# Kernel tuning notes

Hardware: AMD Instinct MI355X
Metric: run time of the kernel (lower is better)

Reference implementation:

```python
import jax, jax.numpy as jnp
import numpy as np
from functools import partial

TAU = 2.0
EPS = 1e-5

@jax.custom_vjp
def spike(x):
    # Heaviside spike (x >= 0 -> 1). Surrogate sigmoid grad (alpha=4), matching spikingjelly default.
    return (x >= 0).astype(x.dtype)

def _spike_fwd(x):
    return (x >= 0).astype(x.dtype), x

def _spike_bwd(x, g):
    s = jax.nn.sigmoid(4.0 * x)
    return (4.0 * s * (1.0 - s) * g,)

spike.defvjp(_spike_fwd, _spike_bwd)

def lif(x, v_threshold=1.0):
    # Multi-step LIF over leading time axis. v_reset=0, hard reset, detach_reset.
    def step(v, xt):
        v = v + (xt - v) / TAU
        s = spike(v - v_threshold)
        v = v * (1.0 - jax.lax.stop_gradient(s))  # detached hard reset
        return v, s
    _, s = jax.lax.scan(step, jnp.zeros_like(x[0]), x)
    return s

def bn(x, gamma, beta):
    # BatchNorm1d in training mode over (T*B, C, N): stats over axes (T,B,N) per channel.
    m = x.mean(axis=(0, 1, 3), keepdims=True)
    v = x.var(axis=(0, 1, 3), keepdims=True)
    return (x - m) * jax.lax.rsqrt(v + EPS) * gamma[None, None, :, None] + beta[None, None, :, None]

def conv1x1(x, w, b=None):
    # 1x1 conv1d == channel-mixing GEMM. x: [T,B,C,N], w: [O,C]
    y = jnp.einsum('oc,tbcn->tbon', w, x)
    if b is not None:
        y = y + b[None, None, :, None]
    return y

def setup_inputs() -> dict:
    key = jax.random.key(0)
    ks = jax.random.split(key, 16)
    T, B, C, H, W = 4, 16, 512, 16, 16
    sc = 1.0 / np.sqrt(C)
    inp = {
        'x': jax.random.normal(ks[0], (T, B, C, H, W), dtype=jnp.float32),
        'q_w': jax.random.normal(ks[1], (C, C), dtype=jnp.float32) * sc,
        'q_gamma': jnp.ones((C,), jnp.float32), 'q_beta': jnp.zeros((C,), jnp.float32),
        'k_w': jax.random.normal(ks[2], (C, C), dtype=jnp.float32) * sc,
        'k_gamma': jnp.ones((C,), jnp.float32), 'k_beta': jnp.zeros((C,), jnp.float32),
        'v_w': jax.random.normal(ks[3], (C, C), dtype=jnp.float32) * sc,
        'v_gamma': jnp.ones((C,), jnp.float32), 'v_beta': jnp.zeros((C,), jnp.float32),
        'proj_w': jax.random.normal(ks[4], (C, C), dtype=jnp.float32) * sc,
        'proj_b': jnp.zeros((C,), jnp.float32),
        'proj_gamma': jnp.ones((C,), jnp.float32), 'proj_beta': jnp.zeros((C,), jnp.float32),
    }
    return inp

def reference(x, q_w, q_gamma, q_beta, k_w, k_gamma, k_beta, v_w, v_gamma, v_beta,
              proj_w, proj_b, proj_gamma, proj_beta):
    num_heads = 8
    scale = 0.125
    T, B, C, H, W = x.shape
    N = H * W
    d = C // num_heads
    xf = x.reshape(T, B, C, N)

    def branch(w, gamma, beta):
        s = lif(bn(conv1x1(xf, w), gamma, beta))          # [T,B,C,N] spikes
        # -> [T,B,heads,N,d]
        return s.transpose(0, 1, 3, 2).reshape(T, B, N, num_heads, d).transpose(0, 1, 3, 2, 4)

    q = branch(q_w, q_gamma, q_beta)
    k = branch(k_w, k_gamma, k_beta)
    v = branch(v_w, v_gamma, v_beta)

    kv = jnp.einsum('tbhnd,tbhne->tbhde', k, v)           # [T,B,h,d,d]
    attn = jnp.einsum('tbhnd,tbhde->tbhne', q, kv) * scale  # [T,B,h,N,d]
    attn = attn.transpose(0, 1, 2, 4, 3).reshape(T, B, C, N)
    attn = lif(attn, v_threshold=0.5)

    out = bn(conv1x1(attn, proj_w, proj_b), proj_gamma, proj_beta)
    out = lif(out.reshape(T, B, C, H, W))
    return out
```

## Files before the change

kernel.cpp:

```cpp
#include <hip/hip_runtime.h>
#include <stdint.h>

#define BCN  (16*512*256)
#define CN   (512*256)
#define NG   64

template<typename IN_T>
__global__ __launch_bounds__(256, 4)
void conv_gemm_v2(const IN_T* __restrict__ X, const float* __restrict__ W,
                  const float* __restrict__ bias, float* __restrict__ Y) {
  const int g  = blockIdx.z;
  const int o0 = blockIdx.y << 7;
  const int n0 = blockIdx.x << 6;
  const int tid = threadIdx.x;
  const int tx = tid & 15, ty = tid >> 4;

  const IN_T* __restrict__ Xg = X + (size_t)g * CN;
  float* __restrict__ Yg = Y + (size_t)g * CN;

  __shared__ double wS[128][33];
  __shared__ double xS[32][66];

  double acc[8][4] = {};

  float wst[16];
  float xst[8];

  auto loadW = [&](int c0) {
    #pragma unroll
    for (int i = 0; i < 4; ++i) {
      int L = i * 256 + tid;
      int o = L >> 3, c4 = (L & 7) << 2;
      const float4 v = *(const float4*)&W[(size_t)(o0 + o) * 512 + c0 + c4];
      wst[4*i+0] = v.x; wst[4*i+1] = v.y; wst[4*i+2] = v.z; wst[4*i+3] = v.w;
    }
  };
  auto loadX = [&](int c0) {
    #pragma unroll
    for (int i = 0; i < 2; ++i) {
      int L = i * 256 + tid;
      int c = L >> 4, n4 = (L & 15) << 2;
      if constexpr (sizeof(IN_T) == 4) {
        const float4 v = *(const float4*)&Xg[(size_t)(c0 + c) * 256 + n0 + n4];
        xst[4*i+0] = v.x; xst[4*i+1] = v.y; xst[4*i+2] = v.z; xst[4*i+3] = v.w;
      } else {
        const uchar4 v = *(const uchar4*)&Xg[(size_t)(c0 + c) * 256 + n0 + n4];
        xst[4*i+0] = (float)v.x; xst[4*i+1] = (float)v.y;
        xst[4*i+2] = (float)v.z; xst[4*i+3] = (float)v.w;
      }
    }
  };
  auto storeTiles = [&]() {
    #pragma unroll
    for (int i = 0; i < 4; ++i) {
      int L = i * 256 + tid;
      int o = L >> 3, c4 = (L & 7) << 2;
      #pragma unroll
      for (int u = 0; u < 4; ++u) wS[o][c4 + u] = (double)wst[4*i+u];
    }
    #pragma unroll
    for (int i = 0; i < 2; ++i) {
      int L = i * 256 + tid;
      int c = L >> 4, n4 = (L & 15) << 2;
      #pragma unroll
      for (int u = 0; u < 4; ++u) xS[c][n4 + u] = (double)xst[4*i+u];
    }
  };

  loadW(0); loadX(0);

  for (int c0 = 0; c0 < 512; c0 += 32) {
    __syncthreads();
    storeTiles();
    __syncthreads();
    if (c0 + 32 < 512) { loadW(c0 + 32); loadX(c0 + 32); }

    #pragma unroll
    for (int k = 0; k < 32; ++k) {
      double b[4];
      #pragma unroll
      for (int j = 0; j < 4; ++j) b[j] = xS[k][tx + 16*j];
      #pragma unroll
      for (int i = 0; i < 8; ++i) {
        double a = wS[ty*8 + i][k];
        #pragma unroll
        for (int j = 0; j < 4; ++j) acc[i][j] = fma(a, b[j], acc[i][j]);
      }
    }
  }

  #pragma unroll
  for (int i = 0; i < 8; ++i) {
    const int o = o0 + ty*8 + i;
    const double bi = bias ? (double)bias[o] : 0.0;
    #pragma unroll
    for (int j = 0; j < 4; ++j)
      Yg[(size_t)o * 256 + n0 + tx + 16*j] = (float)(acc[i][j] + bi);
  }
}

__global__ __launch_bounds__(256)
void bn_stats(const float* __restrict__ Y, const float* __restrict__ gamma,
              const float* __restrict__ beta, double* __restrict__ stats) {
  const int c = blockIdx.x;
  const int tid = threadIdx.x;
  __shared__ double redA[256];
  __shared__ double redB[256];

  double s = 0.0, s2 = 0.0;
  for (int g = 0; g < NG; ++g) {
    double y = (double)Y[((size_t)g * 512 + c) * 256 + tid];
    s += y; s2 += y * y;
  }
  redA[tid] = s; redB[tid] = s2; __syncthreads();
  for (int off = 128; off > 0; off >>= 1) {
    if (tid < off) { redA[tid] += redA[tid + off]; redB[tid] += redB[tid + off]; }
    __syncthreads();
  }
  if (tid == 0) {
    double m = redA[0] * (1.0 / 16384.0);
    double var = redB[0] * (1.0 / 16384.0) - m * m;
    double rstd = 1.0 / sqrt(var + 1e-5);
    double scale = (double)gamma[c] * rstd;
    stats[c] = scale;
    stats[512 + c] = (double)beta[c] - m * scale;
  }
}

__global__ __launch_bounds__(256)
void lif_kernel(const float* __restrict__ Y, const double* __restrict__ stats,
                double thresh, unsigned char* __restrict__ s_u8,
                float* __restrict__ s_f32) {
  const size_t idx = (size_t)blockIdx.x * 256 + threadIdx.x;
  const int c = (int)((idx >> 8) & 511);
  double scale = 1.0, shift = 0.0;
  if (stats) { scale = stats[c]; shift = stats[512 + c]; }
  double v = 0.0;
  #pragma unroll
  for (int t = 0; t < 4; ++t) {
    double z = (double)Y[(size_t)t * BCN + idx] * scale + shift;
    v = v + (z - v) * 0.5;
    bool sp = (v - thresh) >= 0.0;
    if (s_u8) s_u8[(size_t)t * BCN + idx] = sp ? 1 : 0;
    else      s_f32[(size_t)t * BCN + idx] = sp ? 1.0f : 0.0f;
    if (sp) v = 0.0;
  }
}

__global__ __launch_bounds__(256)
void attn_kv(const unsigned char* __restrict__ sk, const unsigned char* __restrict__ sv,
             float* __restrict__ kv) {
  const int blk = blockIdx.x;
  const int tid = threadIdx.x;
  const size_t base = ((size_t)(blk >> 3) * 512 + (size_t)(blk & 7) * 64) * 256;
  __shared__ unsigned char kS[64][256];
  __shared__ unsigned char vS[64][256];
  const uint32_t* K32 = (const uint32_t*)(sk + base);
  const uint32_t* V32 = (const uint32_t*)(sv + base);
  uint32_t* kS32 = (uint32_t*)&kS[0][0];
  uint32_t* vS32 = (uint32_t*)&vS[0][0];
  #pragma unroll
  for (int i = 0; i < 16; ++i) {
    kS32[i * 256 + tid] = K32[i * 256 + tid];
    vS32[i * 256 + tid] = V32[i * 256 + tid];
  }
  __syncthreads();
  const int d0 = (tid >> 4) << 2, e0 = (tid & 15) << 2;
  int acc[4][4] = {};
  for (int n = 0; n < 256; ++n) {
    int k_[4], v_[4];
    #pragma unroll
    for (int i = 0; i < 4; ++i) k_[i] = kS[d0 + i][n];
    #pragma unroll
    for (int j = 0; j < 4; ++j) v_[j] = vS[e0 + j][n];
    #pragma unroll
    for (int i = 0; i < 4; ++i)
      #pragma unroll
      for (int j = 0; j < 4; ++j) acc[i][j] += k_[i] * v_[j];
  }
  float* KV = kv + (size_t)blk * 4096;
  #pragma unroll
  for (int i = 0; i < 4; ++i)
    #pragma unroll
    for (int j = 0; j < 4; ++j)
      KV[(d0 + i) * 64 + e0 + j] = (float)acc[i][j];
}

__global__ __launch_bounds__(256)
void attn_qkv(const unsigned char* __restrict__ sq, const float* __restrict__ kv,
              float* __restrict__ attn) {
  const int blk = blockIdx.x;
  const int tid = threadIdx.x;
  const size_t base = ((size_t)(blk >> 3) * 512 + (size_t)(blk & 7) * 64) * 256;
  __shared__ unsigned char qS[64][256];
  __shared__ float kvS[64][64];
  const uint32_t* Q32 = (const uint32_t*)(sq + base);
  uint32_t* qS32 = (uint32_t*)&qS[0][0];
  const float* KV = kv + (size_t)blk * 4096;
  #pragma unroll
  for (int i = 0; i < 16; ++i) {
    qS32[i * 256 + tid] = Q32[i * 256 + tid];
    (&kvS[0][0])[i * 256 + tid] = KV[i * 256 + tid];
  }
  __syncthreads();
  const int n = tid;
  float acc[64];
  #pragma unroll
  for (int e = 0; e < 64; ++e) acc[e] = 0.0f;
  for (int d = 0; d < 64; ++d) {
    float qf = (float)qS[d][n];
    #pragma unroll
    for (int e = 0; e < 64; ++e) acc[e] = fmaf(qf, kvS[d][e], acc[e]);
  }
  float* A = attn + base;
  #pragma unroll
  for (int e = 0; e < 64; ++e) A[(size_t)e * 256 + n] = acc[e] * 0.125f;
}

extern "C" void kernel_launch(void* const* d_in, const int* in_sizes, int n_in,
                              void* d_out, int out_size, void* d_ws, size_t ws_size,
                              hipStream_t stream) {
  const float* x          = (const float*)d_in[0];
  const float* q_w        = (const float*)d_in[1];
  const float* q_gamma    = (const float*)d_in[2];
  const float* q_beta     = (const float*)d_in[3];
  const float* k_w        = (const float*)d_in[4];
  const float* k_gamma    = (const float*)d_in[5];
  const float* k_beta     = (const float*)d_in[6];
  const float* v_w        = (const float*)d_in[7];
  const float* v_gamma    = (const float*)d_in[8];
  const float* v_beta     = (const float*)d_in[9];
  const float* proj_w     = (const float*)d_in[10];
  const float* proj_b     = (const float*)d_in[11];
  const float* proj_gamma = (const float*)d_in[12];
  const float* proj_beta  = (const float*)d_in[13];

  const size_t YB = (size_t)4 * BCN * sizeof(float);
  const size_t SB = (size_t)4 * BCN;
  if (ws_size < YB + 5 * SB + 1024 * sizeof(double)) return;

  char* ws = (char*)d_ws;
  float* yA           = (float*)ws;
  unsigned char* s_q  = (unsigned char*)(ws + YB);
  unsigned char* s_k  = s_q + SB;
  unsigned char* s_v  = s_k + SB;
  unsigned char* s_at = s_v + SB;
  float* kvb          = (float*)(ws + YB + 4 * SB);
  double* stats       = (double*)(ws + YB + 5 * SB);

  dim3 gGemm(4, 4, NG);

  const float* bw[3] = {q_w, k_w, v_w};
  const float* bg[3] = {q_gamma, k_gamma, v_gamma};
  const float* bb[3] = {q_beta, k_beta, v_beta};
  unsigned char* bs[3] = {s_q, s_k, s_v};

  for (int i = 0; i < 3; ++i) {
    conv_gemm_v2<float><<<gGemm, 256, 0, stream>>>(x, bw[i], nullptr, yA);
    bn_stats<<<512, 256, 0, stream>>>(yA, bg[i], bb[i], stats);
    lif_kernel<<<8192, 256, 0, stream>>>(yA, stats, 1.0, bs[i], nullptr);
  }

  attn_kv<<<512, 256, 0, stream>>>(s_k, s_v, kvb);
  attn_qkv<<<512, 256, 0, stream>>>(s_q, kvb, yA);
  lif_kernel<<<8192, 256, 0, stream>>>(yA, nullptr, 0.5, s_at, nullptr);

  conv_gemm_v2<unsigned char><<<gGemm, 256, 0, stream>>>(s_at, proj_w, proj_b, yA);
  bn_stats<<<512, 256, 0, stream>>>(yA, proj_gamma, proj_beta, stats);
  lif_kernel<<<8192, 256, 0, stream>>>(yA, stats, 1.0, nullptr, (float*)d_out);
}
```

Baseline: 1.058 ms.

## Store GEMM tiles as float in shared memory with transposed weights and vector loads

The conv GEMM now keeps its shared-memory tiles in float instead of double and stores the weight tile transposed (k-major, padded to 132). The inner loop can then read A and B with float4 loads and convert to double in registers, and the output is written with float4 stores. This is meant to halve LDS footprint and traffic and cut the number of shared loads per FMA. In exchange it drops the register prefetch of the next tile, so global loads no longer overlap with compute, and the transposed weight stores may cause bank conflicts.

```diff
diff --git a/kernel.cpp b/kernel.cpp
--- a/kernel.cpp
+++ b/kernel.cpp
@@ -7,95 +7,77 @@
 
 template<typename IN_T>
 __global__ __launch_bounds__(256, 4)
-void conv_gemm_v2(const IN_T* __restrict__ X, const float* __restrict__ W,
+void conv_gemm_v3(const IN_T* __restrict__ X, const float* __restrict__ W,
                   const float* __restrict__ bias, float* __restrict__ Y) {
   const int g  = blockIdx.z;
   const int o0 = blockIdx.y << 7;
   const int n0 = blockIdx.x << 6;
   const int tid = threadIdx.x;
-  const int tx = tid & 15, ty = tid >> 4;
+  const int tx = tid & 15;
+  const int ty = tid >> 4;
 
   const IN_T* __restrict__ Xg = X + (size_t)g * CN;
   float* __restrict__ Yg = Y + (size_t)g * CN;
 
-  __shared__ double wS[128][33];
-  __shared__ double xS[32][66];
+  __shared__ float wT[32 * 132];
+  __shared__ float xT[32 * 64];
 
   double acc[8][4] = {};
 
-  float wst[16];
-  float xst[8];
-
-  auto loadW = [&](int c0) {
+  for (int c0 = 0; c0 < 512; c0 += 32) {
+    __syncthreads();
     #pragma unroll
     for (int i = 0; i < 4; ++i) {
       int L = i * 256 + tid;
-      int o = L >> 3, c4 = (L & 7) << 2;
-      const float4 v = *(const float4*)&W[(size_t)(o0 + o) * 512 + c0 + c4];
-      wst[4*i+0] = v.x; wst[4*i+1] = v.y; wst[4*i+2] = v.z; wst[4*i+3] = v.w;
+      int o = L >> 3, cq = L & 7;
+      const float4 wv = *(const float4*)&W[(size_t)(o0 + o) * 512 + c0 + cq * 4];
+      wT[(cq * 4 + 0) * 132 + o] = wv.x;
+      wT[(cq * 4 + 1) * 132 + o] = wv.y;
+      wT[(cq * 4 + 2) * 132 + o] = wv.z;
+      wT[(cq * 4 + 3) * 132 + o] = wv.w;
     }
-  };
-  auto loadX = [&](int c0) {
     #pragma unroll
     for (int i = 0; i < 2; ++i) {
       int L = i * 256 + tid;
-      int c = L >> 4, n4 = (L & 15) << 2;
+      int k = L >> 4, nq = L & 15;
       if constexpr (sizeof(IN_T) == 4) {
-        const float4 v = *(const float4*)&Xg[(size_t)(c0 + c) * 256 + n0 + n4];
-        xst[4*i+0] = v.x; xst[4*i+1] = v.y; xst[4*i+2] = v.z; xst[4*i+3] = v.w;
+        const float4 xv = *(const float4*)&Xg[(size_t)(c0 + k) * 256 + n0 + nq * 4];
+        *(float4*)&xT[k * 64 + nq * 4] = xv;
       } else {
-        const uchar4 v = *(const uchar4*)&Xg[(size_t)(c0 + c) * 256 + n0 + n4];
-        xst[4*i+0] = (float)v.x; xst[4*i+1] = (float)v.y;
-        xst[4*i+2] = (float)v.z; xst[4*i+3] = (float)v.w;
+        const uchar4 xv = *(const uchar4*)&Xg[(size_t)(c0 + k) * 256 + n0 + nq * 4];
+        float4 xf = make_float4((float)xv.x, (float)xv.y, (float)xv.z, (float)xv.w);
+        *(float4*)&xT[k * 64 + nq * 4] = xf;
       }
     }
-  };
-  auto storeTiles = [&]() {
-    #pragma unroll
-    for (int i = 0; i < 4; ++i) {
-      int L = i * 256 + tid;
-      int o = L >> 3, c4 = (L & 7) << 2;
+    __syncthreads();
+
+    #pragma unroll
+    for (int k = 0; k < 32; ++k) {
+      const float4 A0 = *(const float4*)&wT[k * 132 + ty * 8];
+      const float4 A1 = *(const float4*)&wT[k * 132 + ty * 8 + 4];
+      const float4 B  = *(const float4*)&xT[k * 64 + tx * 4];
+      double a[8], b[4];
+      a[0] = (double)A0.x; a[1] = (double)A0.y; a[2] = (double)A0.z; a[3] = (double)A0.w;
+      a[4] = (double)A1.x; a[5] = (double)A1.y; a[6] = (double)A1.z; a[7] = (double)A1.w;
+      b[0] = (double)B.x;  b[1] = (double)B.y;  b[2] = (double)B.z;  b[3] = (double)B.w;
       #pragma unroll
-      for (int u = 0; u < 4; ++u) wS[o][c4 + u] = (double)wst[4*i+u];
+      for (int i = 0; i < 8; ++i)
+        #pragma unroll
+        for (int j = 0; j < 4; ++j)
+          acc[i][j] = fma(a[i], b[j], acc[i][j]);
     }
-    #pragma unroll
-    for (int i = 0; i < 2; ++i) {
-      int L = i * 256 + tid;
-      int c = L >> 4, n4 = (L & 15) << 2;
-      #pragma unroll
-      for (int u = 0; u < 4; ++u) xS[c][n4 + u] = (double)xst[4*i+u];
-    }
-  };
-
-  loadW(0); loadX(0);
-
-  for (int c0 = 0; c0 < 512; c0 += 32) {
-    __syncthreads();
-    storeTiles();
-    __syncthreads();
-    if (c0 + 32 < 512) { loadW(c0 + 32); loadX(c0 + 32); }
-
-    #pragma unroll
-    for (int k = 0; k < 32; ++k) {
-      double b[4];
-      #pragma unroll
-      for (int j = 0; j < 4; ++j) b[j] = xS[k][tx + 16*j];
-      #pragma unroll
-      for (int i = 0; i < 8; ++i) {
-        double a = wS[ty*8 + i][k];
-        #pragma unroll
-        for (int j = 0; j < 4; ++j) acc[i][j] = fma(a, b[j], acc[i][j]);
-      }
-    }
   }
 
   #pragma unroll
   for (int i = 0; i < 8; ++i) {
-    const int o = o0 + ty*8 + i;
+    const int o = o0 + ty * 8 + i;
     const double bi = bias ? (double)bias[o] : 0.0;
-    #pragma unroll
-    for (int j = 0; j < 4; ++j)
-      Yg[(size_t)o * 256 + n0 + tx + 16*j] = (float)(acc[i][j] + bi);
+    float4 out;
+    out.x = (float)(acc[i][0] + bi);
+    out.y = (float)(acc[i][1] + bi);
+    out.z = (float)(acc[i][2] + bi);
+    out.w = (float)(acc[i][3] + bi);
+    *(float4*)&Yg[(size_t)o * 256 + n0 + tx * 4] = out;
   }
 }
 
@@ -256,7 +238,7 @@
   unsigned char* bs[3] = {s_q, s_k, s_v};
 
   for (int i = 0; i < 3; ++i) {
-    conv_gemm_v2<float><<<gGemm, 256, 0, stream>>>(x, bw[i], nullptr, yA);
+    conv_gemm_v3<float><<<gGemm, 256, 0, stream>>>(x, bw[i], nullptr, yA);
     bn_stats<<<512, 256, 0, stream>>>(yA, bg[i], bb[i], stats);
     lif_kernel<<<8192, 256, 0, stream>>>(yA, stats, 1.0, bs[i], nullptr);
   }
@@ -265,7 +247,7 @@
   attn_qkv<<<512, 256, 0, stream>>>(s_q, kvb, yA);
   lif_kernel<<<8192, 256, 0, stream>>>(yA, nullptr, 0.5, s_at, nullptr);
 
-  conv_gemm_v2<unsigned char><<<gGemm, 256, 0, stream>>>(s_at, proj_w, proj_b, yA);
+  conv_gemm_v3<unsigned char><<<gGemm, 256, 0, stream>>>(s_at, proj_w, proj_b, yA);
   bn_stats<<<512, 256, 0, stream>>>(yA, proj_gamma, proj_beta, stats);
   lif_kernel<<<8192, 256, 0, stream>>>(yA, stats, 1.0, nullptr, (float*)d_out);
 }
```

Result: no change. 1.073 ms (+1.4%).
